# Kernel optimization log

Hardware: AMD Instinct MI355X
Metric: run time of the kernel (lower is better)

Reference implementation:

```python
import jax, jax.numpy as jnp
import numpy as np

D_MODEL = 768
NHEAD = 12
HEAD_DIM = D_MODEL // NHEAD
WINDOW = 33  # band half-width = 16


def setup_inputs() -> dict:
    key = jax.random.key(0)
    ks = jax.random.split(key, 9)
    B, T, C = 2, 4096, D_MODEL
    s = 0.02
    return {
        "x": jax.random.normal(ks[0], (B, T, C), jnp.float32),
        "Wq": jax.random.normal(ks[1], (C, C), jnp.float32) * s,
        "bq": jnp.zeros((C,), jnp.float32),
        "Wk": jax.random.normal(ks[2], (C, C), jnp.float32) * s,
        "bk": jnp.zeros((C,), jnp.float32),
        "Wv": jax.random.normal(ks[3], (C, C), jnp.float32) * s,
        "bv": jnp.zeros((C,), jnp.float32),
        "Wo": jax.random.normal(ks[4], (C, C), jnp.float32) * s,
        "bo": jnp.zeros((C,), jnp.float32),
    }


def reference(x, Wq, bq, Wk, bk, Wv, bv, Wo, bo):
    B, T, C = x.shape
    H, D = NHEAD, HEAD_DIM
    scale = D ** -0.5
    # torch Linear: x @ W.T + b
    q = (x @ Wq.T + bq).reshape(B, T, H, D).transpose(0, 2, 1, 3)  # [B,H,T,D]
    k = (x @ Wk.T + bk).reshape(B, T, H, D).transpose(0, 2, 1, 3)
    v = (x @ Wv.T + bv).reshape(B, T, H, D).transpose(0, 2, 1, 3)
    scores = jnp.einsum("bhqd,bhkd->bhqk", q, k) * scale  # [B,H,T,T]
    idx = jnp.arange(T)
    local_mask = jnp.abs(idx[:, None] - idx[None, :]) <= (WINDOW // 2)  # [T,T]
    scores = jnp.where(local_mask[None, None], scores, -jnp.inf)
    attn = jax.nn.softmax(scores, axis=-1)  # dropout=0 / eval mode
    out = jnp.einsum("bhqk,bhkd->bhqd", attn, v)  # [B,H,T,D]
    out = out.transpose(0, 2, 1, 3).reshape(B, T, C)
    return out @ Wo.T + bo
```

## Files before the change

### kernel.cpp

```cpp
#include <hip/hip_runtime.h>
#include <math.h>
#include <cstdint>
#include <cstddef>

typedef unsigned short u16;
typedef short bf16x8 __attribute__((ext_vector_type(8)));
typedef float f32x4 __attribute__((ext_vector_type(4)));
typedef u16 u16x8 __attribute__((ext_vector_type(8)));
typedef u16 u16x4 __attribute__((ext_vector_type(4)));

#define T_LEN 4096
#define NH 12
#define HD 64
#define DMODEL 768
#define GK 768
#define QKV_STRIDE 6291456ul

__device__ __forceinline__ u16 f2bf(float x) {
  union { float f; unsigned u; } v; v.f = x;
  unsigned r = v.u + 0x7fffu + ((v.u >> 16) & 1u);
  return (u16)(r >> 16);
}
__device__ __forceinline__ float bf2f(u16 x) {
  union { unsigned u; float f; } v; v.u = ((unsigned)x) << 16;
  return v.f;
}
__device__ __forceinline__ void bfpair(unsigned u, float& lo, float& hi) {
  union { unsigned u; float f; } a, b;
  a.u = u << 16; b.u = u & 0xffff0000u;
  lo = a.f; hi = b.f;
}

__device__ __forceinline__ void async16(const u16* g, u16* l) {
  __builtin_amdgcn_global_load_lds(
      (const __attribute__((address_space(1))) unsigned int*)g,
      (__attribute__((address_space(3))) unsigned int*)l, 16, 0, 0);
}

__global__ void cvt_all(const float* __restrict__ x,
                        const float* __restrict__ Wq, const float* __restrict__ Wk,
                        const float* __restrict__ Wv, const float* __restrict__ Wo,
                        u16* __restrict__ xb, u16* __restrict__ wqkv, u16* __restrict__ wo_b) {
  int bx = blockIdx.x;
  const float* s; u16* d; int base;
  if (bx < 6144)      { s = x;  d = xb;             base = bx; }
  else if (bx < 6720) { s = Wq; d = wqkv;           base = bx - 6144; }
  else if (bx < 7296) { s = Wk; d = wqkv + 589824;  base = bx - 6720; }
  else if (bx < 7872) { s = Wv; d = wqkv + 1179648; base = bx - 7296; }
  else                { s = Wo; d = wo_b;           base = bx - 7872; }
  int i = (base * 256 + (int)threadIdx.x) * 4;
  float4 v = *(const float4*)(s + i);
  u16x4 o;
  o[0] = f2bf(v.x); o[1] = f2bf(v.y); o[2] = f2bf(v.z); o[3] = f2bf(v.w);
  *(u16x4*)(d + i) = o;
}

#define BN 128
#define BK 32

template <int EPI, int MI>
__global__ __launch_bounds__(256)
void gemm_bt(const u16* __restrict__ A, const u16* __restrict__ B,
             const float* __restrict__ bias0, const float* __restrict__ bias1,
             const float* __restrict__ bias2, void* __restrict__ outp) {
  constexpr int BMt = MI * 32;
  __shared__ __align__(16) u16 As[BMt * BK];
  __shared__ __align__(16) u16 Bs[BN * BK];

  const int tid  = threadIdx.x;
  const int lane = tid & 63;
  const int wave = tid >> 6;
  const int wm = wave & 1, wn = wave >> 1;
  const long am0 = (long)blockIdx.x * BMt;
  const long bn0 = (long)blockIdx.y * BN;
  const int r16 = lane & 15;
  const int kh  = lane >> 4;
  const int sw8 = (kh ^ ((r16 >> 1) & 3)) * 8;

  f32x4 acc[MI][4] = {};

  const int srow   = lane >> 2;
  const int schunk = ((lane & 3) ^ ((lane >> 3) & 3)) * 8;
  const u16* Ag = A + (am0 + wave * 16 + srow) * GK + schunk;
  const u16* Bg = B + (bn0 + wave * 16 + srow) * GK + schunk;
  u16* Bl0 = &Bs[(wave * 16) * BK];
  u16* Bl1 = &Bs[(64 + wave * 16) * BK];

  for (int kt = 0; kt < GK; kt += BK) {
    __syncthreads();
#pragma unroll
    for (int s = 0; s < MI / 2; s++)
      async16(Ag + (size_t)(s * 64) * GK + kt, &As[(s * 64 + wave * 16) * BK]);
    async16(Bg + kt, Bl0);
    async16(Bg + 64 * GK + kt, Bl1);
    __syncthreads();
    bf16x8 af[MI], bfr[4];
#pragma unroll
    for (int i = 0; i < MI; i++)
      af[i] = *(const bf16x8*)&As[(wm * MI * 16 + i * 16 + r16) * BK + sw8];
#pragma unroll
    for (int j = 0; j < 4; j++)
      bfr[j] = *(const bf16x8*)&Bs[(wn * 64 + j * 16 + r16) * BK + sw8];
#pragma unroll
    for (int i = 0; i < MI; i++)
#pragma unroll
      for (int j = 0; j < 4; j++)
        acc[i][j] = __builtin_amdgcn_mfma_f32_16x16x32_bf16(af[i], bfr[j], acc[i][j], 0, 0, 0);
  }

  const int m0 = (int)am0 + wm * MI * 16;

  if (EPI == 0) {
    const int tens = (int)(bn0 / 768);
    const int c0 = (int)bn0 - tens * 768;
    const float* bp = (tens == 0) ? bias0 : ((tens == 1) ? bias1 : bias2);
    u16* outb = (u16*)outp + (size_t)tens * QKV_STRIDE;
#pragma unroll
    for (int j = 0; j < 4; j++) {
      int col = c0 + wn * 64 + j * 16 + r16;
      float bv = bp[col];
#pragma unroll
      for (int i = 0; i < MI; i++) {
#pragma unroll
        for (int r = 0; r < 4; r++) {
          int row = m0 + i * 16 + kh * 4 + r;
          outb[(size_t)row * DMODEL + col] = f2bf(acc[i][j][r] + bv);
        }
      }
    }
  } else {
    float* O = (float*)outp;
#pragma unroll
    for (int i = 0; i < MI; i++) {
#pragma unroll
      for (int r = 0; r < 4; r++) {
        int row = m0 + i * 16 + kh * 4 + r;
        float* orow = O + (size_t)row * DMODEL;
#pragma unroll
        for (int j = 0; j < 4; j++) {
          int col = (int)bn0 + wn * 64 + j * 16 + r16;
          orow[col] = acc[i][j][r] + bias0[col];
        }
      }
    }
  }
}

#define QB 64
#define SLAB 96
#define KSTR 72

__global__ __launch_bounds__(256)
void attn_local(const u16* __restrict__ qkv, u16* __restrict__ attn) {
  __shared__ __align__(16) u16 Ks[SLAB][KSTR];
  __shared__ __align__(16) u16 Vs[SLAB][KSTR];
  const int tid = threadIdx.x;
  const int q0 = blockIdx.x * QB;
  const int h = blockIdx.y, b = blockIdx.z;
  const size_t rowbase = (size_t)b * T_LEN;
  const int hc = h * HD;
  const u16* Qg = qkv;
  const u16* Kg = qkv + QKV_STRIDE;
  const u16* Vg = qkv + 2 * QKV_STRIDE;

  for (int e = tid; e < SLAB * 8; e += 256) {
    int r = e >> 3, c8 = (e & 7) * 8;
    int g = q0 - 16 + r;
    if (g >= 0 && g < T_LEN) {
      size_t off = (rowbase + g) * DMODEL + hc + c8;
      *(u16x8*)&Ks[r][c8] = *(const u16x8*)(Kg + off);
      *(u16x8*)&Vs[r][c8] = *(const u16x8*)(Vg + off);
    } else {
      u16x8 zz = {0, 0, 0, 0, 0, 0, 0, 0};
      *(u16x8*)&Ks[r][c8] = zz;
      *(u16x8*)&Vs[r][c8] = zz;
    }
  }

  const int qi = tid >> 2;
  const int p  = tid & 3;
  const int d0 = p * 16;
  const int t  = q0 + qi;

  float qv[16];
  {
    const u16* qrow = Qg + (rowbase + t) * DMODEL + hc + d0;
    uint4 a = *(const uint4*)qrow;
    uint4 bq = *(const uint4*)(qrow + 8);
    bfpair(a.x, qv[0], qv[1]);   bfpair(a.y, qv[2], qv[3]);
    bfpair(a.z, qv[4], qv[5]);   bfpair(a.w, qv[6], qv[7]);
    bfpair(bq.x, qv[8], qv[9]);  bfpair(bq.y, qv[10], qv[11]);
    bfpair(bq.z, qv[12], qv[13]); bfpair(bq.w, qv[14], qv[15]);
  }
  __syncthreads();

  float s[33];
#pragma unroll
  for (int j = 0; j < 33; j++) {
    const int row = qi + j;
    uint4 a = *(const uint4*)&Ks[row][d0];
    uint4 c = *(const uint4*)&Ks[row][d0 + 8];
    float k0, k1;
    float a0 = 0.f, a1 = 0.f;
    bfpair(a.x, k0, k1); a0 += qv[0] * k0;  a1 += qv[1] * k1;
    bfpair(a.y, k0, k1); a0 += qv[2] * k0;  a1 += qv[3] * k1;
    bfpair(a.z, k0, k1); a0 += qv[4] * k0;  a1 += qv[5] * k1;
    bfpair(a.w, k0, k1); a0 += qv[6] * k0;  a1 += qv[7] * k1;
    bfpair(c.x, k0, k1); a0 += qv[8] * k0;  a1 += qv[9] * k1;
    bfpair(c.y, k0, k1); a0 += qv[10] * k0; a1 += qv[11] * k1;
    bfpair(c.z, k0, k1); a0 += qv[12] * k0; a1 += qv[13] * k1;
    bfpair(c.w, k0, k1); a0 += qv[14] * k0; a1 += qv[15] * k1;
    float sc = a0 + a1;
    sc += __shfl_xor(sc, 1);
    sc += __shfl_xor(sc, 2);
    int kidx = t - 16 + j;
    s[j] = (kidx >= 0 && kidx < T_LEN) ? sc * 0.125f : -INFINITY;
  }

  float m = s[0];
#pragma unroll
  for (int j = 1; j < 33; j++) m = fmaxf(m, s[j]);
  float l = 0.f;
#pragma unroll
  for (int j = 0; j < 33; j++) {
    float pp = __expf(s[j] - m);
    s[j] = pp;
    l += pp;
  }
  float inv = 1.0f / l;

  float o[16] = {};
#pragma unroll
  for (int j = 0; j < 33; j++) {
    const int row = qi + j;
    float pp = s[j];
    uint4 a = *(const uint4*)&Vs[row][d0];
    uint4 c = *(const uint4*)&Vs[row][d0 + 8];
    float v0, v1;
    bfpair(a.x, v0, v1); o[0]  += pp * v0; o[1]  += pp * v1;
    bfpair(a.y, v0, v1); o[2]  += pp * v0; o[3]  += pp * v1;
    bfpair(a.z, v0, v1); o[4]  += pp * v0; o[5]  += pp * v1;
    bfpair(a.w, v0, v1); o[6]  += pp * v0; o[7]  += pp * v1;
    bfpair(c.x, v0, v1); o[8]  += pp * v0; o[9]  += pp * v1;
    bfpair(c.y, v0, v1); o[10] += pp * v0; o[11] += pp * v1;
    bfpair(c.z, v0, v1); o[12] += pp * v0; o[13] += pp * v1;
    bfpair(c.w, v0, v1); o[14] += pp * v0; o[15] += pp * v1;
  }

  u16* orow = attn + (rowbase + t) * DMODEL + hc + d0;
  u16x8 ov;
#pragma unroll
  for (int z = 0; z < 8; z++) ov[z] = f2bf(o[z] * inv);
  *(u16x8*)orow = ov;
#pragma unroll
  for (int z = 0; z < 8; z++) ov[z] = f2bf(o[8 + z] * inv);
  *(u16x8*)(orow + 8) = ov;
}

extern "C" void kernel_launch(void* const* d_in, const int* in_sizes, int n_in,
                              void* d_out, int out_size, void* d_ws, size_t ws_size,
                              hipStream_t stream) {
  const float* x  = (const float*)d_in[0];
  const float* Wq = (const float*)d_in[1];
  const float* bq = (const float*)d_in[2];
  const float* Wk = (const float*)d_in[3];
  const float* bk = (const float*)d_in[4];
  const float* Wv = (const float*)d_in[5];
  const float* bv = (const float*)d_in[6];
  const float* Wo = (const float*)d_in[7];
  const float* bo = (const float*)d_in[8];
  float* out = (float*)d_out;
  char* ws = (char*)d_ws;

  u16* xb   = (u16*)(ws);
  u16* wqkv = (u16*)(ws + 12582912);
  u16* wo_b = (u16*)(ws + 16121856);
  u16* qkv  = (u16*)(ws + 17301504);
  u16* attn = (u16*)(ws + 55050240);

  cvt_all<<<8448, 256, 0, stream>>>(x, Wq, Wk, Wv, Wo, xb, wqkv, wo_b);

  gemm_bt<0, 4><<<dim3(64, 18), 256, 0, stream>>>(xb, wqkv, bq, bk, bv, (void*)qkv);
  attn_local<<<dim3(64, 12, 2), 256, 0, stream>>>(qkv, attn);
  gemm_bt<1, 2><<<dim3(128, 6), 256, 0, stream>>>(attn, wo_b, bo, bo, bo, (void*)out);
}
```

Before: 187.3 us.

## Compute banded attention with MFMA and store V in tiled transposed layout

Replaces the scalar per-thread banded attention with a wave-level MFMA kernel that computes 16x48 score tiles, does the softmax with lane shuffles, stages probabilities in LDS and multiplies them with V via MFMA. The QKV GEMM epilogue now writes V in a per-head tiled transposed layout so the PV operand can be loaded directly as MFMA fragments. This is meant to remove the FMA-bound scalar dot products and the LDS K/V slab staging. It risks scattered 2-byte stores in the V epilogue and out-of-range reads at sequence edges that rely on masking and zero probabilities.

```diff
diff --git a/kernel.cpp b/kernel.cpp
--- a/kernel.cpp
+++ b/kernel.cpp
@@ -20,15 +20,6 @@
   union { float f; unsigned u; } v; v.f = x;
   unsigned r = v.u + 0x7fffu + ((v.u >> 16) & 1u);
   return (u16)(r >> 16);
-}
-__device__ __forceinline__ float bf2f(u16 x) {
-  union { unsigned u; float f; } v; v.u = ((unsigned)x) << 16;
-  return v.f;
-}
-__device__ __forceinline__ void bfpair(unsigned u, float& lo, float& hi) {
-  union { unsigned u; float f; } a, b;
-  a.u = u << 16; b.u = u & 0xffff0000u;
-  lo = a.f; hi = b.f;
 }
 
 __device__ __forceinline__ void async16(const u16* g, u16* l) {
@@ -114,17 +105,38 @@
     const int tens = (int)(bn0 / 768);
     const int c0 = (int)bn0 - tens * 768;
     const float* bp = (tens == 0) ? bias0 : ((tens == 1) ? bias1 : bias2);
-    u16* outb = (u16*)outp + (size_t)tens * QKV_STRIDE;
-#pragma unroll
-    for (int j = 0; j < 4; j++) {
-      int col = c0 + wn * 64 + j * 16 + r16;
-      float bv = bp[col];
-#pragma unroll
-      for (int i = 0; i < MI; i++) {
-#pragma unroll
-        for (int r = 0; r < 4; r++) {
-          int row = m0 + i * 16 + kh * 4 + r;
-          outb[(size_t)row * DMODEL + col] = f2bf(acc[i][j][r] + bv);
+    if (tens < 2) {
+      u16* outb = (u16*)outp + (size_t)tens * QKV_STRIDE;
+#pragma unroll
+      for (int j = 0; j < 4; j++) {
+        int col = c0 + wn * 64 + j * 16 + r16;
+        float bv = bp[col];
+#pragma unroll
+        for (int i = 0; i < MI; i++) {
+#pragma unroll
+          for (int r = 0; r < 4; r++) {
+            int row = m0 + i * 16 + kh * 4 + r;
+            outb[(size_t)row * DMODEL + col] = f2bf(acc[i][j][r] + bv);
+          }
+        }
+      }
+    } else {
+      u16* vtb = (u16*)outp + 2 * QKV_STRIDE;
+#pragma unroll
+      for (int j = 0; j < 4; j++) {
+        int cl = c0 + wn * 64 + j * 16;
+        int hj = cl >> 6, dbase = cl & 63;
+        float bv = bp[cl + r16];
+#pragma unroll
+        for (int i = 0; i < MI; i++) {
+#pragma unroll
+          for (int r = 0; r < 4; r++) {
+            int row = m0 + i * 16 + kh * 4 + r;
+            int b_ = row >> 12, t = row & 4095;
+            size_t addr = (((size_t)(b_ * NH + hj) * 256 + (t >> 4)) << 10)
+                          + (size_t)(dbase + r16) * 16 + (t & 15);
+            vtb[addr] = f2bf(acc[i][j][r] + bv);
+          }
         }
       }
     }
@@ -146,115 +158,104 @@
   }
 }
 
-#define QB 64
-#define SLAB 96
-#define KSTR 72
+#define PSS 72
 
 __global__ __launch_bounds__(256)
-void attn_local(const u16* __restrict__ qkv, u16* __restrict__ attn) {
-  __shared__ __align__(16) u16 Ks[SLAB][KSTR];
-  __shared__ __align__(16) u16 Vs[SLAB][KSTR];
-  const int tid = threadIdx.x;
-  const int q0 = blockIdx.x * QB;
+void attn_mfma(const u16* __restrict__ qkv, const u16* __restrict__ vt,
+               u16* __restrict__ attn) {
+  __shared__ __align__(16) u16 Ps[4][16 * PSS];
+  const int tid = threadIdx.x, lane = tid & 63, wave = tid >> 6;
+  const int r16 = lane & 15, quad = lane >> 4;
+  const int q0 = blockIdx.x * 64;
   const int h = blockIdx.y, b = blockIdx.z;
-  const size_t rowbase = (size_t)b * T_LEN;
+  const long rowbase = (long)b * T_LEN;
   const int hc = h * HD;
   const u16* Qg = qkv;
   const u16* Kg = qkv + QKV_STRIDE;
-  const u16* Vg = qkv + 2 * QKV_STRIDE;
-
-  for (int e = tid; e < SLAB * 8; e += 256) {
-    int r = e >> 3, c8 = (e & 7) * 8;
-    int g = q0 - 16 + r;
-    if (g >= 0 && g < T_LEN) {
-      size_t off = (rowbase + g) * DMODEL + hc + c8;
-      *(u16x8*)&Ks[r][c8] = *(const u16x8*)(Kg + off);
-      *(u16x8*)&Vs[r][c8] = *(const u16x8*)(Vg + off);
-    } else {
-      u16x8 zz = {0, 0, 0, 0, 0, 0, 0, 0};
-      *(u16x8*)&Ks[r][c8] = zz;
-      *(u16x8*)&Vs[r][c8] = zz;
-    }
-  }
-
-  const int qi = tid >> 2;
-  const int p  = tid & 3;
-  const int d0 = p * 16;
-  const int t  = q0 + qi;
-
-  float qv[16];
-  {
-    const u16* qrow = Qg + (rowbase + t) * DMODEL + hc + d0;
-    uint4 a = *(const uint4*)qrow;
-    uint4 bq = *(const uint4*)(qrow + 8);
-    bfpair(a.x, qv[0], qv[1]);   bfpair(a.y, qv[2], qv[3]);
-    bfpair(a.z, qv[4], qv[5]);   bfpair(a.w, qv[6], qv[7]);
-    bfpair(bq.x, qv[8], qv[9]);  bfpair(bq.y, qv[10], qv[11]);
-    bfpair(bq.z, qv[12], qv[13]); bfpair(bq.w, qv[14], qv[15]);
-  }
-  __syncthreads();
-
-  float s[33];
-#pragma unroll
-  for (int j = 0; j < 33; j++) {
-    const int row = qi + j;
-    uint4 a = *(const uint4*)&Ks[row][d0];
-    uint4 c = *(const uint4*)&Ks[row][d0 + 8];
-    float k0, k1;
-    float a0 = 0.f, a1 = 0.f;
-    bfpair(a.x, k0, k1); a0 += qv[0] * k0;  a1 += qv[1] * k1;
-    bfpair(a.y, k0, k1); a0 += qv[2] * k0;  a1 += qv[3] * k1;
-    bfpair(a.z, k0, k1); a0 += qv[4] * k0;  a1 += qv[5] * k1;
-    bfpair(a.w, k0, k1); a0 += qv[6] * k0;  a1 += qv[7] * k1;
-    bfpair(c.x, k0, k1); a0 += qv[8] * k0;  a1 += qv[9] * k1;
-    bfpair(c.y, k0, k1); a0 += qv[10] * k0; a1 += qv[11] * k1;
-    bfpair(c.z, k0, k1); a0 += qv[12] * k0; a1 += qv[13] * k1;
-    bfpair(c.w, k0, k1); a0 += qv[14] * k0; a1 += qv[15] * k1;
-    float sc = a0 + a1;
-    sc += __shfl_xor(sc, 1);
-    sc += __shfl_xor(sc, 2);
-    int kidx = t - 16 + j;
-    s[j] = (kidx >= 0 && kidx < T_LEN) ? sc * 0.125f : -INFINITY;
-  }
-
-  float m = s[0];
-#pragma unroll
-  for (int j = 1; j < 33; j++) m = fmaxf(m, s[j]);
-  float l = 0.f;
-#pragma unroll
-  for (int j = 0; j < 33; j++) {
-    float pp = __expf(s[j] - m);
-    s[j] = pp;
-    l += pp;
-  }
-  float inv = 1.0f / l;
-
-  float o[16] = {};
-#pragma unroll
-  for (int j = 0; j < 33; j++) {
-    const int row = qi + j;
-    float pp = s[j];
-    uint4 a = *(const uint4*)&Vs[row][d0];
-    uint4 c = *(const uint4*)&Vs[row][d0 + 8];
-    float v0, v1;
-    bfpair(a.x, v0, v1); o[0]  += pp * v0; o[1]  += pp * v1;
-    bfpair(a.y, v0, v1); o[2]  += pp * v0; o[3]  += pp * v1;
-    bfpair(a.z, v0, v1); o[4]  += pp * v0; o[5]  += pp * v1;
-    bfpair(a.w, v0, v1); o[6]  += pp * v0; o[7]  += pp * v1;
-    bfpair(c.x, v0, v1); o[8]  += pp * v0; o[9]  += pp * v1;
-    bfpair(c.y, v0, v1); o[10] += pp * v0; o[11] += pp * v1;
-    bfpair(c.z, v0, v1); o[12] += pp * v0; o[13] += pp * v1;
-    bfpair(c.w, v0, v1); o[14] += pp * v0; o[15] += pp * v1;
-  }
-
-  u16* orow = attn + (rowbase + t) * DMODEL + hc + d0;
-  u16x8 ov;
-#pragma unroll
-  for (int z = 0; z < 8; z++) ov[z] = f2bf(o[z] * inv);
-  *(u16x8*)orow = ov;
-#pragma unroll
-  for (int z = 0; z < 8; z++) ov[z] = f2bf(o[8 + z] * inv);
-  *(u16x8*)(orow + 8) = ov;
+  const u16* Vh = vt + ((size_t)(b * NH + h)) * (256 * 1024);
+
+  const int qbase = q0 + wave * 16;
+  const int kb = qbase - 16;
+
+  const u16* qrow = Qg + (rowbase + qbase + r16) * DMODEL + hc + quad * 8;
+  bf16x8 qa0 = *(const bf16x8*)qrow;
+  bf16x8 qa1 = *(const bf16x8*)(qrow + 32);
+
+  f32x4 s[3];
+#pragma unroll
+  for (int t = 0; t < 3; t++) {
+    const u16* krow = Kg + (rowbase + kb + t * 16 + r16) * DMODEL + hc + quad * 8;
+    bf16x8 kf0 = *(const bf16x8*)krow;
+    bf16x8 kf1 = *(const bf16x8*)(krow + 32);
+    f32x4 a = {};
+    a = __builtin_amdgcn_mfma_f32_16x16x32_bf16(qa0, kf0, a, 0, 0, 0);
+    a = __builtin_amdgcn_mfma_f32_16x16x32_bf16(qa1, kf1, a, 0, 0, 0);
+    s[t] = a;
+  }
+
+  float pr[3][4];
+#pragma unroll
+  for (int r = 0; r < 4; r++) {
+    const int qg = qbase + quad * 4 + r;
+    float sc[3];
+#pragma unroll
+    for (int t = 0; t < 3; t++) {
+      int key = kb + t * 16 + r16;
+      bool ok = (key >= qg - 16) && (key <= qg + 16) && (key >= 0) && (key < T_LEN);
+      sc[t] = ok ? s[t][r] * 0.125f : -INFINITY;
+    }
+    float mx = fmaxf(sc[0], fmaxf(sc[1], sc[2]));
+    mx = fmaxf(mx, __shfl_xor(mx, 1));
+    mx = fmaxf(mx, __shfl_xor(mx, 2));
+    mx = fmaxf(mx, __shfl_xor(mx, 4));
+    mx = fmaxf(mx, __shfl_xor(mx, 8));
+    float e0 = __expf(sc[0] - mx), e1 = __expf(sc[1] - mx), e2 = __expf(sc[2] - mx);
+    float l = e0 + e1 + e2;
+    l += __shfl_xor(l, 1);
+    l += __shfl_xor(l, 2);
+    l += __shfl_xor(l, 4);
+    l += __shfl_xor(l, 8);
+    float inv = 1.0f / l;
+    pr[0][r] = e0 * inv; pr[1][r] = e1 * inv; pr[2][r] = e2 * inv;
+  }
+
+  u16* psw = &Ps[wave][0];
+#pragma unroll
+  for (int t = 0; t < 3; t++)
+#pragma unroll
+    for (int r = 0; r < 4; r++)
+      psw[(quad * 4 + r) * PSS + t * 16 + r16] = f2bf(pr[t][r]);
+#pragma unroll
+  for (int r = 0; r < 4; r++)
+    psw[(quad * 4 + r) * PSS + 48 + r16] = 0;
+
+  bf16x8 pa0 = *(const bf16x8*)&psw[r16 * PSS + quad * 8];
+  bf16x8 pa1 = *(const bf16x8*)&psw[r16 * PSS + 32 + quad * 8];
+
+  const int kq1 = kb + quad * 8;
+  const int kq2 = kb + 32 + quad * 8;
+  const int o1 = (kq1 >> 4) * 1024 + (kq1 & 15);
+  const int o2 = (kq2 >> 4) * 1024 + (kq2 & 15);
+  f32x4 o[4];
+#pragma unroll
+  for (int c = 0; c < 4; c++) {
+    const u16* vb = Vh + (16 * c + r16) * 16;
+    bf16x8 v1 = *(const bf16x8*)(vb + o1);
+    bf16x8 v2 = *(const bf16x8*)(vb + o2);
+    f32x4 a = {};
+    a = __builtin_amdgcn_mfma_f32_16x16x32_bf16(pa0, v1, a, 0, 0, 0);
+    a = __builtin_amdgcn_mfma_f32_16x16x32_bf16(pa1, v2, a, 0, 0, 0);
+    o[c] = a;
+  }
+
+#pragma unroll
+  for (int c = 0; c < 4; c++) {
+#pragma unroll
+    for (int r = 0; r < 4; r++) {
+      int qg = qbase + quad * 4 + r;
+      attn[(rowbase + qg) * DMODEL + hc + 16 * c + r16] = f2bf(o[c][r]);
+    }
+  }
 }
 
 extern "C" void kernel_launch(void* const* d_in, const int* in_sizes, int n_in,
@@ -281,6 +282,6 @@
   cvt_all<<<8448, 256, 0, stream>>>(x, Wq, Wk, Wv, Wo, xb, wqkv, wo_b);
 
   gemm_bt<0, 4><<<dim3(64, 18), 256, 0, stream>>>(xb, wqkv, bq, bk, bv, (void*)qkv);
-  attn_local<<<dim3(64, 12, 2), 256, 0, stream>>>(qkv, attn);
+  attn_mfma<<<dim3(64, 12, 2), 256, 0, stream>>>(qkv, qkv + 2 * QKV_STRIDE, attn);
   gemm_bt<1, 2><<<dim3(128, 6), 256, 0, stream>>>(attn, wo_b, bo, bo, bo, (void*)out);
 }
```

Measured after the change: 177.4 us. 1.06x faster.
